# Performance work log

Hardware: AMD Instinct MI355X
Metric: run time of the kernel (lower is better)

The kernel has to match this reference:

```python
import jax, jax.numpy as jnp
import numpy as np

MAX_ITERS = 256  # matches init_kwargs max_iters


def setup_inputs() -> dict:
    key = jax.random.key(0)
    k1, k2 = jax.random.split(key)
    H = W = 4096
    # classic Mandelbrot viewing window
    c_real = jax.random.uniform(k1, (H, W), jnp.float32, -2.0, 0.5)
    c_imag = jax.random.uniform(k2, (H, W), jnp.float32, -1.25, 1.25)
    return {"c_real": c_real, "c_imag": c_imag}


def reference(c_real, c_imag):
    # z starts at c (NOT zero), as in the torch module
    zr0 = c_real
    zi0 = c_imag
    active0 = jnp.ones(c_real.shape, dtype=bool)
    counts0 = jnp.full(c_real.shape, float(MAX_ITERS), dtype=c_real.dtype)

    def body(step, state):
        zr, zi, active, counts = state
        escaped_now = active & (zr * zr + zi * zi >= 4.0)
        counts = jnp.where(escaped_now, step.astype(counts.dtype), counts)
        active = active & ~escaped_now
        # torch loop only updates z for step < max_iters
        do_update = active & (step < MAX_ITERS)
        next_real = zr * zr - zi * zi + c_real
        next_imag = 2.0 * zr * zi + c_imag
        zr = jnp.where(do_update, next_real, zr)
        zi = jnp.where(do_update, next_imag, zi)
        return (zr, zi, active, counts)

    _, _, _, counts = jax.lax.fori_loop(
        0, MAX_ITERS + 1, body, (zr0, zi0, active0, counts0)
    )
    return counts
```

## Files before the change

kernel.cpp:

```cpp
#include <hip/hip_runtime.h>


#define MAX_ITERS 256

typedef __attribute__((ext_vector_type(2))) float f32x2;
typedef __attribute__((ext_vector_type(4))) float f32x4;

__device__ __forceinline__ float mul32(float a, float b) {
    float d; asm("v_mul_f32 %0, %1, %2" : "=v"(d) : "v"(a), "v"(b)); return d;
}
__device__ __forceinline__ float add32(float a, float b) {
    float d; asm("v_add_f32 %0, %1, %2" : "=v"(d) : "v"(a), "v"(b)); return d;
}
__device__ __forceinline__ float fma32(float a, float b, float c) {
    float d; asm("v_fma_f32 %0, %1, %2, %3" : "=v"(d) : "v"(a), "v"(b), "v"(c)); return d;
}
__device__ __forceinline__ float fma32_negc(float a, float b, float c) {
    float d; asm("v_fma_f32 %0, %1, %2, -%3" : "=v"(d) : "v"(a), "v"(b), "v"(c)); return d;
}

__device__ __forceinline__ void iter_checks(float cr, float ci,
                                            float& zr, float& zi,
                                            float& act, float& cnt, int nchecks)
{
    #pragma unroll 8
    for (int s = 0; s < nchecks; ++s) {
        const float zi2 = mul32(zi, zi);
        const float mag = fma32(zr, zr, zi2);
        act = (mag < 4.0f) ? act : 0.0f;
        cnt = cnt + act;
        const float t   = fma32_negc(zr, zr, zi2);
        const float nr  = add32(t, cr);
        const float t2  = add32(zr, zr);
        zi = fma32(t2, zi, ci);
        zr = nr;
    }
}

__device__ __forceinline__ void zstep2(const f32x2 cr, const f32x2 ci,
                                       f32x2& zr, f32x2& zi, f32x2& mag)
{
    f32x2 s, t, u;
    asm("v_pk_mul_f32 %0, %5, %5\n\t"
        "v_pk_fma_f32 %1, %4, %4, %0\n\t"
        "v_pk_fma_f32 %2, %4, %4, %0 neg_lo:[0,0,1] neg_hi:[0,0,1]\n\t"
        "v_pk_add_f32 %3, %4, %4\n\t"
        "v_pk_add_f32 %4, %2, %6\n\t"
        "v_pk_fma_f32 %5, %3, %5, %7"
        : "=&v"(s), "=&v"(mag), "=&v"(t), "=&v"(u), "+v"(zr), "+v"(zi)
        : "v"(cr), "v"(ci));
}

__device__ __forceinline__ void check4(
    const f32x2 crA, const f32x2 ciA, f32x2& zrA, f32x2& ziA,
    const f32x2 crB, const f32x2 ciB, f32x2& zrB, f32x2& ziB,
    float& act0, float& act1, float& act2, float& act3,
    float& cnt0, float& cnt1, float& cnt2, float& cnt3)
{
    f32x2 magA, magB;
    zstep2(crA, ciA, zrA, ziA, magA);
    zstep2(crB, ciB, zrB, ziB, magB);
    act0 = (magA.x < 4.0f) ? act0 : 0.0f;  cnt0 += act0;
    act1 = (magA.y < 4.0f) ? act1 : 0.0f;  cnt1 += act1;
    act2 = (magB.x < 4.0f) ? act2 : 0.0f;  cnt2 += act2;
    act3 = (magB.y < 4.0f) ? act3 : 0.0f;  cnt3 += act3;
}

__device__ __forceinline__ int lane_id() {
    return __builtin_amdgcn_mbcnt_hi(~0u, __builtin_amdgcn_mbcnt_lo(~0u, 0));
}

__device__ __forceinline__ bool in_shortcut(float cr, float ci) {
    const float xq = cr - 0.25f;
    const float q  = xq * xq + ci * ci;
    const bool in_card = (q * (q + xq) - 0.25f * ci * ci) < -1e-3f;
    const float xb = cr + 1.0f;
    const bool in_bulb = (xb * xb + ci * ci) < (0.0625f - 1e-3f);
    return in_card | in_bulb;
}

__device__ __forceinline__ void phaseA_quad(
    const float* __restrict__ c_real, const float* __restrict__ c_imag,
    float* __restrict__ out, unsigned char* __restrict__ ws,
    unsigned seg_cap, int n, int p0, int seg)
{
    if (p0 + 3 >= n) {
        for (int j = 0; j < 4 && p0 + j < n; ++j) {
            const float cr = c_real[p0 + j], ci = c_imag[p0 + j];
            if (in_shortcut(cr, ci)) { out[p0 + j] = 256.0f; continue; }
            float zr = cr, zi = ci, act = 1.0f, cnt = 0.0f;
            iter_checks(cr, ci, zr, zi, act, cnt, MAX_ITERS);
            out[p0 + j] = cnt;
        }
        return;
    }

    const f32x4 cr4 = *(const f32x4*)(c_real + p0);
    const f32x4 ci4 = *(const f32x4*)(c_imag + p0);
    const f32x2 crA = {cr4.x, cr4.y}, ciA = {ci4.x, ci4.y};
    const f32x2 crB = {cr4.z, cr4.w}, ciB = {ci4.z, ci4.w};
    const bool sc0 = in_shortcut(cr4.x, ci4.x);
    const bool sc1 = in_shortcut(cr4.y, ci4.y);
    const bool sc2 = in_shortcut(cr4.z, ci4.z);
    const bool sc3 = in_shortcut(cr4.w, ci4.w);

    f32x2 zrA = crA, ziA = ciA, zrB = crB, ziB = ciB;
    float act0 = 1.0f, act1 = 1.0f, act2 = 1.0f, act3 = 1.0f;
    float cnt0 = 0.0f, cnt1 = 0.0f, cnt2 = 0.0f, cnt3 = 0.0f;
    #pragma unroll
    for (int s = 0; s < 16; ++s)
        check4(crA, ciA, zrA, ziA, crB, ciB, zrB, ziB,
               act0, act1, act2, act3, cnt0, cnt1, cnt2, cnt3);

    const bool sv0 = (!sc0) && (act0 != 0.0f);
    const bool sv1 = (!sc1) && (act1 != 0.0f);
    const bool sv2 = (!sc2) && (act2 != 0.0f);
    const bool sv3 = (!sc3) && (act3 != 0.0f);

    const unsigned long long m0 = __ballot(sv0);
    const unsigned long long m1 = __ballot(sv1);
    const unsigned long long m2 = __ballot(sv2);
    const unsigned long long m3 = __ballot(sv3);
    const unsigned long long any = m0 | m1 | m2 | m3;
    if (any != 0ull) {
        const int lane = lane_id();
        const int leader = (int)__ffsll(any) - 1;
        unsigned* ctr = (unsigned*)(ws + (size_t)seg * 64u);
        const unsigned c0 = (unsigned)__popcll(m0);
        const unsigned c1 = (unsigned)__popcll(m1);
        const unsigned c2 = (unsigned)__popcll(m2);
        unsigned base = 0u;
        if (lane == leader)
            base = atomicAdd(ctr, c0 + c1 + c2 + (unsigned)__popcll(m3));
        base = (unsigned)__shfl((int)base, leader, 64);
        float4* qf = (float4*)(ws + 4096);
        int*    qi = (int*)(ws + 4096 + (size_t)seg_cap * 64u * 16u);
        const unsigned long long below = (1ull << lane) - 1ull;
        const size_t segbase = (size_t)seg * seg_cap;

        float zrv[4] = {zrA.x, zrA.y, zrB.x, zrB.y};
        float ziv[4] = {ziA.x, ziA.y, ziB.x, ziB.y};
        float crv[4] = {cr4.x, cr4.y, cr4.z, cr4.w};
        float civ[4] = {ci4.x, ci4.y, ci4.z, ci4.w};
        float cnv[4] = {cnt0, cnt1, cnt2, cnt3};
        const bool svv[4] = {sv0, sv1, sv2, sv3};
        const unsigned prev[4] = {0u, c0, c0 + c1, c0 + c1 + c2};
        const unsigned long long mv[4] = {m0, m1, m2, m3};
        #pragma unroll
        for (int j = 0; j < 4; ++j) {
            if (!svv[j]) continue;
            const unsigned slot = base + prev[j] +
                (unsigned)__popcll(mv[j] & below);
            if (slot < seg_cap) {
                qf[segbase + slot] = make_float4(zrv[j], ziv[j], crv[j], civ[j]);
                qi[segbase + slot] = p0 + j;
            } else {
                float zrs = zrv[j], zis = ziv[j], as = 1.0f, cs = cnv[j];
                iter_checks(crv[j], civ[j], zrs, zis, as, cs, 240);
                out[p0 + j] = cs;
            }
        }
    }
    if (!sv0) out[p0 + 0] = sc0 ? 256.0f : cnt0;
    if (!sv1) out[p0 + 1] = sc1 ? 256.0f : cnt1;
    if (!sv2) out[p0 + 2] = sc2 ? 256.0f : cnt2;
    if (!sv3) out[p0 + 3] = sc3 ? 256.0f : cnt3;
}

template <int NCHECKS, int START, bool HAS_DST>
__device__ __forceinline__ void strip_phase(
    float* __restrict__ out, unsigned char* __restrict__ ws,
    const float4* __restrict__ srcF, const int* __restrict__ srcI,
    float4* __restrict__ dstF, int* __restrict__ dstI,
    int src_ctr, int dst_ctr, unsigned seg_cap,
    int seg, int grp, int blocks_per_seg)
{
    const unsigned cnt_s = __hip_atomic_load(
        (const unsigned*)(ws + (size_t)seg * 64u + (size_t)src_ctr * 4u),
        __ATOMIC_RELAXED, __HIP_MEMORY_SCOPE_AGENT);
    const unsigned nq = (cnt_s < seg_cap) ? cnt_s : seg_cap;
    const unsigned q = (nq + 3u) >> 2;
    const unsigned stride = (unsigned)blocks_per_seg * 256u;
    const size_t segbase = (size_t)seg * seg_cap;
    const int lane = lane_id();

    for (unsigned k = (unsigned)grp * 256u + threadIdx.x; k < q; k += stride) {
        const unsigned i1 = k + q, i2 = k + 2u * q, i3 = k + 3u * q;
        const bool v1 = (i1 < nq), v2 = (i2 < nq), v3 = (i3 < nq);
        const float4 r0 = srcF[segbase + k];
        const float4 r1 = v1 ? srcF[segbase + i1] : r0;
        const float4 r2 = v2 ? srcF[segbase + i2] : r0;
        const float4 r3 = v3 ? srcF[segbase + i3] : r0;
        const int idx0 = srcI[segbase + k];
        const int idx1 = v1 ? srcI[segbase + i1] : -1;
        const int idx2 = v2 ? srcI[segbase + i2] : -1;
        const int idx3 = v3 ? srcI[segbase + i3] : -1;

        f32x2 zrA = {r0.x, r1.x}, ziA = {r0.y, r1.y};
        f32x2 crA = {r0.z, r1.z}, ciA = {r0.w, r1.w};
        f32x2 zrB = {r2.x, r3.x}, ziB = {r2.y, r3.y};
        f32x2 crB = {r2.z, r3.z}, ciB = {r2.w, r3.w};
        float act0 = 1.0f, act1 = v1 ? 1.0f : 0.0f;
        float act2 = v2 ? 1.0f : 0.0f, act3 = v3 ? 1.0f : 0.0f;
        float cnt0 = (float)START, cnt1 = (float)START;
        float cnt2 = (float)START, cnt3 = (float)START;
        #pragma unroll 8
        for (int s = 0; s < NCHECKS; ++s)
            check4(crA, ciA, zrA, ziA, crB, ciB, zrB, ziB,
                   act0, act1, act2, act3, cnt0, cnt1, cnt2, cnt3);

        if (HAS_DST) {
            const bool sv0 = (act0 != 0.0f);
            const bool sv1 = (act1 != 0.0f);
            const bool sv2 = (act2 != 0.0f);
            const bool sv3 = (act3 != 0.0f);
            const unsigned long long m0 = __ballot(sv0);
            const unsigned long long m1 = __ballot(sv1);
            const unsigned long long m2 = __ballot(sv2);
            const unsigned long long m3 = __ballot(sv3);
            const unsigned long long any = m0 | m1 | m2 | m3;
            if (any != 0ull) {
                const int leader = (int)__ffsll(any) - 1;
                unsigned* ctr = (unsigned*)(ws + (size_t)seg * 64u
                                               + (size_t)dst_ctr * 4u);
                const unsigned c0 = (unsigned)__popcll(m0);
                const unsigned c1 = (unsigned)__popcll(m1);
                const unsigned c2 = (unsigned)__popcll(m2);
                unsigned base = 0u;
                if (lane == leader)
                    base = atomicAdd(ctr, c0 + c1 + c2 + (unsigned)__popcll(m3));
                base = (unsigned)__shfl((int)base, leader, 64);
                const unsigned long long below = (1ull << lane) - 1ull;

                float zrv[4] = {zrA.x, zrA.y, zrB.x, zrB.y};
                float ziv[4] = {ziA.x, ziA.y, ziB.x, ziB.y};
                float crv[4] = {crA.x, crA.y, crB.x, crB.y};
                float civ[4] = {ciA.x, ciA.y, ciB.x, ciB.y};
                float cnv[4] = {cnt0, cnt1, cnt2, cnt3};
                const int  idxv[4] = {idx0, idx1, idx2, idx3};
                const bool svv[4] = {sv0, sv1, sv2, sv3};
                const unsigned prev[4] = {0u, c0, c0 + c1, c0 + c1 + c2};
                const unsigned long long mv[4] = {m0, m1, m2, m3};
                #pragma unroll
                for (int j = 0; j < 4; ++j) {
                    if (!svv[j]) continue;
                    const unsigned slot = base + prev[j] +
                        (unsigned)__popcll(mv[j] & below);
                    if (slot < seg_cap) {
                        dstF[segbase + slot] =
                            make_float4(zrv[j], ziv[j], crv[j], civ[j]);
                        dstI[segbase + slot] = idxv[j];
                    } else {
                        float zrs = zrv[j], zis = ziv[j], as = 1.0f, cs = cnv[j];
                        iter_checks(crv[j], civ[j], zrs, zis, as, cs,
                                    256 - START - NCHECKS);
                        out[idxv[j]] = cs;
                    }
                }
            }
            if (!sv0) out[idx0] = cnt0;
            if (v1 && !sv1) out[idx1] = cnt1;
            if (v2 && !sv2) out[idx2] = cnt2;
            if (v3 && !sv3) out[idx3] = cnt3;
        } else {
            out[idx0] = cnt0;
            if (v1) out[idx1] = cnt1;
            if (v2) out[idx2] = cnt2;
            if (v3) out[idx3] = cnt3;
        }
    }
}

__global__ __launch_bounds__(256) void mandel_stage_a_q(
    const float* __restrict__ c_real, const float* __restrict__ c_imag,
    float* __restrict__ out, unsigned char* __restrict__ ws,
    unsigned seg_cap, int n)
{
    const int tq = blockIdx.x * blockDim.x + threadIdx.x;
    const int p0 = tq << 2;
    if (p0 >= n) return;
    phaseA_quad(c_real, c_imag, out, ws, seg_cap, n, p0, blockIdx.x & 63);
}

template <int NCHECKS, int START, bool HAS_DST>
__global__ __launch_bounds__(256) void mandel_strip_q(
    float* __restrict__ out, unsigned char* __restrict__ ws,
    const float4* __restrict__ srcF, const int* __restrict__ srcI,
    float4* __restrict__ dstF, int* __restrict__ dstI,
    int src_ctr, int dst_ctr, unsigned seg_cap, int blocks_per_seg)
{
    strip_phase<NCHECKS, START, HAS_DST>(
        out, ws, srcF, srcI, dstF, dstI, src_ctr, dst_ctr, seg_cap,
        (int)(blockIdx.x & 63u), (int)(blockIdx.x >> 6), blocks_per_seg);
}

__global__ __launch_bounds__(256) void mandel_mono(
    const float* __restrict__ c_real, const float* __restrict__ c_imag,
    float* __restrict__ out, int n)
{
    int i = blockIdx.x * blockDim.x + threadIdx.x;
    if (i >= n) return;
    const float cr = c_real[i], ci = c_imag[i];
    float zr = cr, zi = ci, act = 1.0f, cnt = 0.0f;
    iter_checks(cr, ci, zr, zi, act, cnt, MAX_ITERS);
    out[i] = cnt;
}

extern "C" void kernel_launch(void* const* d_in, const int* in_sizes, int n_in,
                              void* d_out, int out_size, void* d_ws, size_t ws_size,
                              hipStream_t stream)
{
    const float* c_real = (const float*)d_in[0];
    const float* c_imag = (const float*)d_in[1];
    float* out = (float*)d_out;
    const int n = in_sizes[0];
    const int block = 256;

    unsigned char* ws = (unsigned char*)d_ws;
    const size_t avail = (ws_size > 4096) ? (ws_size - 4096) : 0;
    const unsigned seg_cap1 = (unsigned)(avail / (64u * 20u));
    const unsigned seg_cap2 = (unsigned)(avail / (64u * 20u * 2u));

    if (seg_cap1 < 8192u) {
        const int gridA = (n + block - 1) / block;
        mandel_mono<<<gridA, block, 0, stream>>>(c_real, c_imag, out, n);
        return;
    }

    hipMemsetAsync(ws, 0, 4096, stream);

    const int nquads = (n + 3) / 4;
    const int gridA = (nquads + block - 1) / block;

    if (seg_cap2 >= 33000u) {
        const unsigned sc = seg_cap2;
        float4* q0f = (float4*)(ws + 4096);
        int*    q0i = (int*)(ws + 4096 + (size_t)sc * 64u * 16u);
        float4* q1f = (float4*)(ws + 4096 + (size_t)sc * 64u * 20u);
        int*    q1i = (int*)(ws + 4096 + (size_t)sc * 64u * 20u
                                       + (size_t)sc * 64u * 16u);

        mandel_stage_a_q<<<gridA, block, 0, stream>>>(c_real, c_imag, out,
                                                      ws, sc, n);
        mandel_strip_q<40, 16, true><<<64 * 32, block, 0, stream>>>(
            out, ws, q0f, q0i, q1f, q1i, 0, 1, sc, 32);
        mandel_strip_q<80, 56, true><<<64 * 16, block, 0, stream>>>(
            out, ws, q1f, q1i, q0f, q0i, 1, 2, sc, 16);
        mandel_strip_q<120, 136, false><<<64 * 16, block, 0, stream>>>(
            out, ws, q0f, q0i, (float4*)nullptr, (int*)nullptr, 2, 0, sc, 16);
        return;
    }

    mandel_stage_a_q<<<gridA, block, 0, stream>>>(c_real, c_imag, out,
                                                  ws, seg_cap1, n);
    mandel_strip_q<240, 16, false><<<64 * 32, block, 0, stream>>>(
        out, ws,
        (const float4*)(ws + 4096),
        (const int*)(ws + 4096 + (size_t)seg_cap1 * 64u * 16u),
        (float4*)nullptr, (int*)nullptr, 0, 0, seg_cap1, 32);
}
```

Baseline: 239.0 us.

## Process eight pixels per thread in stage A and merge strip passes into two

After: 363.2 us. 1.52x slower.

```diff
diff --git a/kernel.cpp b/kernel.cpp
--- a/kernel.cpp
+++ b/kernel.cpp
@@ -79,13 +79,17 @@
     return in_card | in_bulb;
 }
 
-__device__ __forceinline__ void phaseA_quad(
+__global__ __launch_bounds__(256) void mandel_stage_a_o(
     const float* __restrict__ c_real, const float* __restrict__ c_imag,
     float* __restrict__ out, unsigned char* __restrict__ ws,
-    unsigned seg_cap, int n, int p0, int seg)
-{
-    if (p0 + 3 >= n) {
-        for (int j = 0; j < 4 && p0 + j < n; ++j) {
+    unsigned seg_cap, int n)
+{
+    const int to = blockIdx.x * blockDim.x + threadIdx.x;
+    const int p0 = to << 3;
+    if (p0 >= n) return;
+
+    if (p0 + 7 >= n) {
+        for (int j = 0; j < 8 && p0 + j < n; ++j) {
             const float cr = c_real[p0 + j], ci = c_imag[p0 + j];
             if (in_shortcut(cr, ci)) { out[p0 + j] = 256.0f; continue; }
             float zr = cr, zi = ci, act = 1.0f, cnt = 0.0f;
@@ -95,86 +99,102 @@
         return;
     }
 
-    const f32x4 cr4 = *(const f32x4*)(c_real + p0);
-    const f32x4 ci4 = *(const f32x4*)(c_imag + p0);
-    const f32x2 crA = {cr4.x, cr4.y}, ciA = {ci4.x, ci4.y};
-    const f32x2 crB = {cr4.z, cr4.w}, ciB = {ci4.z, ci4.w};
-    const bool sc0 = in_shortcut(cr4.x, ci4.x);
-    const bool sc1 = in_shortcut(cr4.y, ci4.y);
-    const bool sc2 = in_shortcut(cr4.z, ci4.z);
-    const bool sc3 = in_shortcut(cr4.w, ci4.w);
+    const f32x4 crL = *(const f32x4*)(c_real + p0);
+    const f32x4 crH = *(const f32x4*)(c_real + p0 + 4);
+    const f32x4 ciL = *(const f32x4*)(c_imag + p0);
+    const f32x4 ciH = *(const f32x4*)(c_imag + p0 + 4);
+    const f32x2 crA = {crL.x, crL.y}, crB = {crL.z, crL.w};
+    const f32x2 crC = {crH.x, crH.y}, crD = {crH.z, crH.w};
+    const f32x2 ciA = {ciL.x, ciL.y}, ciB = {ciL.z, ciL.w};
+    const f32x2 ciC = {ciH.x, ciH.y}, ciD = {ciH.z, ciH.w};
+
+    const bool sc[8] = {
+        in_shortcut(crA.x, ciA.x), in_shortcut(crA.y, ciA.y),
+        in_shortcut(crB.x, ciB.x), in_shortcut(crB.y, ciB.y),
+        in_shortcut(crC.x, ciC.x), in_shortcut(crC.y, ciC.y),
+        in_shortcut(crD.x, ciD.x), in_shortcut(crD.y, ciD.y)};
 
     f32x2 zrA = crA, ziA = ciA, zrB = crB, ziB = ciB;
-    float act0 = 1.0f, act1 = 1.0f, act2 = 1.0f, act3 = 1.0f;
-    float cnt0 = 0.0f, cnt1 = 0.0f, cnt2 = 0.0f, cnt3 = 0.0f;
+    f32x2 zrC = crC, ziC = ciC, zrD = crD, ziD = ciD;
+    float a0 = 1.0f, a1 = 1.0f, a2 = 1.0f, a3 = 1.0f;
+    float a4 = 1.0f, a5 = 1.0f, a6 = 1.0f, a7 = 1.0f;
+    float n0 = 0.0f, n1 = 0.0f, n2 = 0.0f, n3 = 0.0f;
+    float n4 = 0.0f, n5 = 0.0f, n6 = 0.0f, n7 = 0.0f;
+
     #pragma unroll
-    for (int s = 0; s < 16; ++s)
+    for (int it = 0; it < 16; ++it) {
         check4(crA, ciA, zrA, ziA, crB, ciB, zrB, ziB,
-               act0, act1, act2, act3, cnt0, cnt1, cnt2, cnt3);
-
-    const bool sv0 = (!sc0) && (act0 != 0.0f);
-    const bool sv1 = (!sc1) && (act1 != 0.0f);
-    const bool sv2 = (!sc2) && (act2 != 0.0f);
-    const bool sv3 = (!sc3) && (act3 != 0.0f);
-
-    const unsigned long long m0 = __ballot(sv0);
-    const unsigned long long m1 = __ballot(sv1);
-    const unsigned long long m2 = __ballot(sv2);
-    const unsigned long long m3 = __ballot(sv3);
-    const unsigned long long any = m0 | m1 | m2 | m3;
+               a0, a1, a2, a3, n0, n1, n2, n3);
+        check4(crC, ciC, zrC, ziC, crD, ciD, zrD, ziD,
+               a4, a5, a6, a7, n4, n5, n6, n7);
+    }
+
+    const float av[8] = {a0, a1, a2, a3, a4, a5, a6, a7};
+    const float nv[8] = {n0, n1, n2, n3, n4, n5, n6, n7};
+    bool sv[8];
+    #pragma unroll
+    for (int j = 0; j < 8; ++j) sv[j] = (!sc[j]) && (av[j] != 0.0f);
+
+    unsigned long long mv[8];
+    unsigned long long any = 0ull;
+    #pragma unroll
+    for (int j = 0; j < 8; ++j) { mv[j] = __ballot(sv[j]); any |= mv[j]; }
+
+    const int lane = lane_id();
     if (any != 0ull) {
-        const int lane = lane_id();
         const int leader = (int)__ffsll(any) - 1;
+        const int seg = blockIdx.x & 63;
         unsigned* ctr = (unsigned*)(ws + (size_t)seg * 64u);
-        const unsigned c0 = (unsigned)__popcll(m0);
-        const unsigned c1 = (unsigned)__popcll(m1);
-        const unsigned c2 = (unsigned)__popcll(m2);
+        unsigned prev[8], tot = 0u;
+        #pragma unroll
+        for (int j = 0; j < 8; ++j) {
+            prev[j] = tot; tot += (unsigned)__popcll(mv[j]);
+        }
         unsigned base = 0u;
-        if (lane == leader)
-            base = atomicAdd(ctr, c0 + c1 + c2 + (unsigned)__popcll(m3));
+        if (lane == leader) base = atomicAdd(ctr, tot);
         base = (unsigned)__shfl((int)base, leader, 64);
         float4* qf = (float4*)(ws + 4096);
         int*    qi = (int*)(ws + 4096 + (size_t)seg_cap * 64u * 16u);
         const unsigned long long below = (1ull << lane) - 1ull;
         const size_t segbase = (size_t)seg * seg_cap;
 
-        float zrv[4] = {zrA.x, zrA.y, zrB.x, zrB.y};
-        float ziv[4] = {ziA.x, ziA.y, ziB.x, ziB.y};
-        float crv[4] = {cr4.x, cr4.y, cr4.z, cr4.w};
-        float civ[4] = {ci4.x, ci4.y, ci4.z, ci4.w};
-        float cnv[4] = {cnt0, cnt1, cnt2, cnt3};
-        const bool svv[4] = {sv0, sv1, sv2, sv3};
-        const unsigned prev[4] = {0u, c0, c0 + c1, c0 + c1 + c2};
-        const unsigned long long mv[4] = {m0, m1, m2, m3};
+        const float zrv[8] = {zrA.x, zrA.y, zrB.x, zrB.y,
+                              zrC.x, zrC.y, zrD.x, zrD.y};
+        const float ziv[8] = {ziA.x, ziA.y, ziB.x, ziB.y,
+                              ziC.x, ziC.y, ziD.x, ziD.y};
+        const float crv[8] = {crA.x, crA.y, crB.x, crB.y,
+                              crC.x, crC.y, crD.x, crD.y};
+        const float civ[8] = {ciA.x, ciA.y, ciB.x, ciB.y,
+                              ciC.x, ciC.y, ciD.x, ciD.y};
         #pragma unroll
-        for (int j = 0; j < 4; ++j) {
-            if (!svv[j]) continue;
+        for (int j = 0; j < 8; ++j) {
+            if (!sv[j]) continue;
             const unsigned slot = base + prev[j] +
                 (unsigned)__popcll(mv[j] & below);
             if (slot < seg_cap) {
                 qf[segbase + slot] = make_float4(zrv[j], ziv[j], crv[j], civ[j]);
                 qi[segbase + slot] = p0 + j;
             } else {
-                float zrs = zrv[j], zis = ziv[j], as = 1.0f, cs = cnv[j];
+                float zrs = zrv[j], zis = ziv[j], as = 1.0f, cs = nv[j];
                 iter_checks(crv[j], civ[j], zrs, zis, as, cs, 240);
                 out[p0 + j] = cs;
             }
         }
     }
-    if (!sv0) out[p0 + 0] = sc0 ? 256.0f : cnt0;
-    if (!sv1) out[p0 + 1] = sc1 ? 256.0f : cnt1;
-    if (!sv2) out[p0 + 2] = sc2 ? 256.0f : cnt2;
-    if (!sv3) out[p0 + 3] = sc3 ? 256.0f : cnt3;
+    #pragma unroll
+    for (int j = 0; j < 8; ++j)
+        if (!sv[j]) out[p0 + j] = sc[j] ? 256.0f : nv[j];
 }
 
 template <int NCHECKS, int START, bool HAS_DST>
-__device__ __forceinline__ void strip_phase(
+__global__ __launch_bounds__(256) void mandel_strip_q(
     float* __restrict__ out, unsigned char* __restrict__ ws,
     const float4* __restrict__ srcF, const int* __restrict__ srcI,
     float4* __restrict__ dstF, int* __restrict__ dstI,
-    int src_ctr, int dst_ctr, unsigned seg_cap,
-    int seg, int grp, int blocks_per_seg)
-{
+    int src_ctr, int dst_ctr, unsigned seg_cap, int blocks_per_seg)
+{
+    const int seg = (int)(blockIdx.x & 63u);
+    const int grp = (int)(blockIdx.x >> 6);
     const unsigned cnt_s = __hip_atomic_load(
         (const unsigned*)(ws + (size_t)seg * 64u + (size_t)src_ctr * 4u),
         __ATOMIC_RELAXED, __HIP_MEMORY_SCOPE_AGENT);
@@ -232,20 +252,20 @@
                 base = (unsigned)__shfl((int)base, leader, 64);
                 const unsigned long long below = (1ull << lane) - 1ull;
 
-                float zrv[4] = {zrA.x, zrA.y, zrB.x, zrB.y};
-                float ziv[4] = {ziA.x, ziA.y, ziB.x, ziB.y};
-                float crv[4] = {crA.x, crA.y, crB.x, crB.y};
-                float civ[4] = {ciA.x, ciA.y, ciB.x, ciB.y};
-                float cnv[4] = {cnt0, cnt1, cnt2, cnt3};
+                const float zrv[4] = {zrA.x, zrA.y, zrB.x, zrB.y};
+                const float ziv[4] = {ziA.x, ziA.y, ziB.x, ziB.y};
+                const float crv[4] = {crA.x, crA.y, crB.x, crB.y};
+                const float civ[4] = {ciA.x, ciA.y, ciB.x, ciB.y};
+                const float cnv[4] = {cnt0, cnt1, cnt2, cnt3};
                 const int  idxv[4] = {idx0, idx1, idx2, idx3};
                 const bool svv[4] = {sv0, sv1, sv2, sv3};
                 const unsigned prev[4] = {0u, c0, c0 + c1, c0 + c1 + c2};
-                const unsigned long long mv[4] = {m0, m1, m2, m3};
+                const unsigned long long mvv[4] = {m0, m1, m2, m3};
                 #pragma unroll
                 for (int j = 0; j < 4; ++j) {
                     if (!svv[j]) continue;
                     const unsigned slot = base + prev[j] +
-                        (unsigned)__popcll(mv[j] & below);
+                        (unsigned)__popcll(mvv[j] & below);
                     if (slot < seg_cap) {
                         dstF[segbase + slot] =
                             make_float4(zrv[j], ziv[j], crv[j], civ[j]);
@@ -271,29 +291,6 @@
     }
 }
 
-__global__ __launch_bounds__(256) void mandel_stage_a_q(
-    const float* __restrict__ c_real, const float* __restrict__ c_imag,
-    float* __restrict__ out, unsigned char* __restrict__ ws,
-    unsigned seg_cap, int n)
-{
-    const int tq = blockIdx.x * blockDim.x + threadIdx.x;
-    const int p0 = tq << 2;
-    if (p0 >= n) return;
-    phaseA_quad(c_real, c_imag, out, ws, seg_cap, n, p0, blockIdx.x & 63);
-}
-
-template <int NCHECKS, int START, bool HAS_DST>
-__global__ __launch_bounds__(256) void mandel_strip_q(
-    float* __restrict__ out, unsigned char* __restrict__ ws,
-    const float4* __restrict__ srcF, const int* __restrict__ srcI,
-    float4* __restrict__ dstF, int* __restrict__ dstI,
-    int src_ctr, int dst_ctr, unsigned seg_cap, int blocks_per_seg)
-{
-    strip_phase<NCHECKS, START, HAS_DST>(
-        out, ws, srcF, srcI, dstF, dstI, src_ctr, dst_ctr, seg_cap,
-        (int)(blockIdx.x & 63u), (int)(blockIdx.x >> 6), blocks_per_seg);
-}
-
 __global__ __launch_bounds__(256) void mandel_mono(
     const float* __restrict__ c_real, const float* __restrict__ c_imag,
     float* __restrict__ out, int n)
@@ -329,8 +326,8 @@
 
     hipMemsetAsync(ws, 0, 4096, stream);
 
-    const int nquads = (n + 3) / 4;
-    const int gridA = (nquads + block - 1) / block;
+    const int nocts = (n + 7) / 8;
+    const int gridA = (nocts + block - 1) / block;
 
     if (seg_cap2 >= 33000u) {
         const unsigned sc = seg_cap2;
@@ -340,18 +337,16 @@
         int*    q1i = (int*)(ws + 4096 + (size_t)sc * 64u * 20u
                                        + (size_t)sc * 64u * 16u);
 
-        mandel_stage_a_q<<<gridA, block, 0, stream>>>(c_real, c_imag, out,
+        mandel_stage_a_o<<<gridA, block, 0, stream>>>(c_real, c_imag, out,
                                                       ws, sc, n);
-        mandel_strip_q<40, 16, true><<<64 * 32, block, 0, stream>>>(
+        mandel_strip_q<70, 16, true><<<64 * 32, block, 0, stream>>>(
             out, ws, q0f, q0i, q1f, q1i, 0, 1, sc, 32);
-        mandel_strip_q<80, 56, true><<<64 * 16, block, 0, stream>>>(
-            out, ws, q1f, q1i, q0f, q0i, 1, 2, sc, 16);
-        mandel_strip_q<120, 136, false><<<64 * 16, block, 0, stream>>>(
-            out, ws, q0f, q0i, (float4*)nullptr, (int*)nullptr, 2, 0, sc, 16);
+        mandel_strip_q<170, 86, false><<<64 * 16, block, 0, stream>>>(
+            out, ws, q1f, q1i, (float4*)nullptr, (int*)nullptr, 1, 0, sc, 16);
         return;
     }
 
-    mandel_stage_a_q<<<gridA, block, 0, stream>>>(c_real, c_imag, out,
+    mandel_stage_a_o<<<gridA, block, 0, stream>>>(c_real, c_imag, out,
                                                   ws, seg_cap1, n);
     mandel_strip_q<240, 16, false><<<64 * 32, block, 0, stream>>>(
         out, ws,
```
